# Optimization experiments

Measured on AMD Instinct MI355X. Metric: run time of the kernel, lower is better.

## Reference

```python
import jax, jax.numpy as jnp
import numpy as np

EMBED_DIM = 1024
N_HEADS = 16
DK = EMBED_DIM // N_HEADS


def setup_inputs() -> dict:
    key = jax.random.key(0)
    ks = jax.random.split(key, 9)
    s = 1.0 / np.sqrt(EMBED_DIM)
    d = EMBED_DIM
    return {
        "x": jax.random.normal(ks[0], (2, 2048, d), dtype=jnp.float32),
        "Wq": jax.random.uniform(ks[1], (d, d), jnp.float32, -s, s),
        "bq": jax.random.uniform(ks[2], (d,), jnp.float32, -s, s),
        "Wk": jax.random.uniform(ks[3], (d, d), jnp.float32, -s, s),
        "bk": jax.random.uniform(ks[4], (d,), jnp.float32, -s, s),
        "Wv": jax.random.uniform(ks[5], (d, d), jnp.float32, -s, s),
        "bv": jax.random.uniform(ks[6], (d,), jnp.float32, -s, s),
        "Wo": jax.random.uniform(ks[7], (d, d), jnp.float32, -s, s),
        "bo": jax.random.uniform(ks[8], (d,), jnp.float32, -s, s),
    }


def reference(x, Wq, bq, Wk, bk, Wv, bv, Wo, bo):
    B, S, D = x.shape
    H, dk = N_HEADS, DK
    # QKV projections
    q = (x @ Wq + bq).reshape(B, S, H, dk).transpose(0, 2, 1, 3)  # [B,H,S,dk]
    k = (x @ Wk + bk).reshape(B, S, H, dk).transpose(0, 2, 1, 3)
    v = (x @ Wv + bv).reshape(B, S, H, dk).transpose(0, 2, 1, 3)
    # scaled dot-product attention with full score matrix (faithful to source)
    scores = jnp.einsum("bhqd,bhkd->bhqk", q, k) / jnp.sqrt(jnp.float32(dk))
    attn = jax.nn.softmax(scores, axis=-1)
    out = jnp.einsum("bhqk,bhkd->bhqd", attn, v)  # [B,H,S,dk]
    out = out.transpose(0, 2, 1, 3).reshape(B, S, D)
    return out @ Wo + bo
```

## Files before the change

kernel.cpp:

```cpp
#include <hip/hip_runtime.h>

typedef unsigned short u16;
typedef unsigned int u32;
typedef __attribute__((ext_vector_type(8))) short short8;
typedef __attribute__((ext_vector_type(4))) float float4v;
typedef __attribute__((ext_vector_type(4))) unsigned int uint4v;

struct alignas(8) U16x4 { u16 x, y, z, w; };

__device__ __forceinline__ u16 f2b(float f) {
    union { float f; unsigned int u; } v; v.f = f;
    unsigned int r = (v.u >> 16) & 1u;
    v.u += 0x7fffu + r;
    return (u16)(v.u >> 16);
}

__device__ __forceinline__ float b2f(u16 u) {
    union { unsigned int u; float f; } v; v.u = ((u32)u) << 16; return v.f;
}

__device__ __forceinline__ u32 cvt_pk_bf16(float lo, float hi) {
    u32 d;
    asm("v_cvt_pk_bf16_f32 %0, %1, %2" : "=v"(d) : "v"(lo), "v"(hi));
    return d;
}

__device__ __forceinline__ void gld16(const u16* g, u16* l) {
    __builtin_amdgcn_global_load_lds(
        (const __attribute__((address_space(1))) void*)g,
        (__attribute__((address_space(3))) void*)l, 16, 0, 0);
}

__device__ __forceinline__ short8 frag8(const u16* base, int row, int cg) {
    return *(const short8*)(base + row * 64 + ((cg ^ (row & 7)) << 3));
}

__global__ __launch_bounds__(256) void prep_kernel(
    const float* __restrict__ x, const float* __restrict__ W0,
    const float* __restrict__ W1, const float* __restrict__ W2,
    const float* __restrict__ W3, u16* __restrict__ xb,
    u16* __restrict__ T0, u16* __restrict__ T1,
    u16* __restrict__ T2, u16* __restrict__ T3) {
    __shared__ float tile[32][33];
    int id = blockIdx.x;
    if (id < 4096) {
        size_t i = ((size_t)id * 256 + threadIdx.x) * 4;
        float4 v = *(const float4*)(x + i);
        U16x4 o;
        o.x = f2b(v.x); o.y = f2b(v.y); o.z = f2b(v.z); o.w = f2b(v.w);
        *(U16x4*)(xb + i) = o;
        return;
    }
    int r = id - 4096;
    int z = r >> 10, tl = r & 1023;
    const float* W = (z == 0) ? W0 : (z == 1) ? W1 : (z == 2) ? W2 : W3;
    u16* T = (z == 0) ? T0 : (z == 1) ? T1 : (z == 2) ? T2 : T3;
    int t = threadIdx.x;
    int tx = t & 31, ty = t >> 5;
    int bn = (tl & 31) * 32, bk = (tl >> 5) * 32;
#pragma unroll
    for (int p = 0; p < 4; ++p) {
        int k = ty + p * 8;
        tile[k][tx] = W[(size_t)(bk + k) * 1024 + bn + tx];
    }
    __syncthreads();
#pragma unroll
    for (int p = 0; p < 4; ++p) {
        int n = ty + p * 8;
        T[(size_t)(bn + n) * 1024 + bk + tx] = f2b(tile[tx][n]);
    }
}

__global__ __launch_bounds__(512, 4) void qkv_kernel(
    const u16* __restrict__ X,
    const u16* __restrict__ WqT, const u16* __restrict__ WkT, const u16* __restrict__ WvT,
    const float* __restrict__ bq, const float* __restrict__ bk, const float* __restrict__ bv,
    u16* __restrict__ Qo, u16* __restrict__ Ko, u16* __restrict__ VTo) {
    __shared__ __align__(16) u16 As[64 * 64];
    __shared__ __align__(16) u16 Bs[3][128 * 64];
    int id = blockIdx.x;
    int m = (id & 7) | (((id >> 3) & 7) << 3);
    int n = id >> 6;
    int t = threadIdx.x;
    int m0 = m * 64, n0 = n * 128;
    int lane = t & 63, wid = t >> 6;
    int l16 = lane & 15, quad = lane >> 4;
    int rl = lane >> 3, cs = lane & 7;

    int z_st = (wid - 2) >> 1, half = wid & 1;
    const u16* gsrcB = (z_st == 0) ? WqT : (z_st == 1) ? WkT : WvT;

    float4v acc[3][4];
    float4v zero4 = {0.f, 0.f, 0.f, 0.f};
#pragma unroll
    for (int z = 0; z < 3; ++z)
#pragma unroll
        for (int i = 0; i < 4; ++i) acc[z][i] = zero4;

    for (int k0 = 0; k0 < 1024; k0 += 64) {
        __syncthreads();
        if (wid < 2) {
#pragma unroll
            for (int p = 0; p < 4; ++p) {
                int q = wid * 4 + p;
                int row = q * 8 + rl;
                int c = cs ^ (row & 7);
                gld16(X + (size_t)(m0 + row) * 1024 + k0 + c * 8, As + q * 512);
            }
        } else {
#pragma unroll
            for (int p = 0; p < 8; ++p) {
                int q = half * 8 + p;
                int row = q * 8 + rl;
                int c = cs ^ (row & 7);
                gld16(gsrcB + (size_t)(n0 + row) * 1024 + k0 + c * 8,
                      &Bs[z_st][0] + q * 512);
            }
        }
        __syncthreads();
#pragma unroll
        for (int ks = 0; ks < 64; ks += 32) {
            int cg = (ks >> 3) + quad;
            short8 af[4];
#pragma unroll
            for (int i = 0; i < 4; ++i)
                af[i] = frag8(As, i * 16 + l16, cg);
#pragma unroll
            for (int z = 0; z < 3; ++z) {
                short8 bf = frag8(&Bs[z][0], wid * 16 + l16, cg);
#pragma unroll
                for (int i = 0; i < 4; ++i)
                    acc[z][i] = __builtin_amdgcn_mfma_f32_16x16x32_bf16(
                        af[i], bf, acc[z][i], 0, 0, 0);
            }
        }
    }

    const float QSCALE = 0.18033688011112042f;
    int n1 = n0 + wid * 16 + l16;
    float bql = bq[n1], bkl = bk[n1], bvl = bv[n1];
#pragma unroll
    for (int i = 0; i < 4; ++i) {
        int mbase = m0 + i * 16 + quad * 4;
#pragma unroll
        for (int r = 0; r < 4; ++r) {
            Qo[(size_t)(mbase + r) * 1024 + n1] =
                f2b((acc[0][i][r] + bql) * QSCALE);
            Ko[(size_t)(mbase + r) * 1024 + n1] =
                f2b(acc[1][i][r] + bkl);
        }
        int bidx = mbase >> 11, s = mbase & 2047;
        size_t base =
            ((size_t)((bidx * 16 + (n1 >> 6)) * 64 + (n1 & 63))) * 2048 + s;
        U16x4 pk;
        pk.x = f2b(acc[2][i][0] + bvl);
        pk.y = f2b(acc[2][i][1] + bvl);
        pk.z = f2b(acc[2][i][2] + bvl);
        pk.w = f2b(acc[2][i][3] + bvl);
        *(U16x4*)(VTo + base) = pk;
    }
}

__global__ __launch_bounds__(256, 4) void oproj_kernel(const u16* __restrict__ Op,
                                                       const float* __restrict__ lp,
                                                       const u16* __restrict__ WoT,
                                                       const float* __restrict__ bias,
                                                       float* __restrict__ out) {
    __shared__ __align__(16) u16 As[64 * 64];
    __shared__ __align__(16) u16 Bs[64 * 64];
    __shared__ float invs[64][16];
    int id = blockIdx.x;
    int m = (id & 7) | (((id >> 3) & 7) << 3);
    int n = id >> 6;
    int t = threadIdx.x;
    int m0 = m * 64, n0 = n * 64;
    int lane = t & 63, wid = t >> 6;
    int l16 = lane & 15, quad = lane >> 4;
    int rl = lane >> 3, cs = lane & 7;

#pragma unroll
    for (int e = t; e < 1024; e += 256) {
        int row = e >> 4, h = e & 15;
        int qg = (m0 + row) * 16 + h;
        invs[row][h] = 1.0f / (lp[qg] + lp[65536 + qg]);
    }

    float4v acc[4];
    float4v zero4 = {0.f, 0.f, 0.f, 0.f};
#pragma unroll
    for (int i = 0; i < 4; ++i) acc[i] = zero4;

    for (int k0 = 0; k0 < 1024; k0 += 64) {
        __syncthreads();
#pragma unroll
        for (int p = 0; p < 2; ++p) {
            int blk = wid * 2 + p;
            int row = blk * 8 + rl;
            int c = cs ^ (row & 7);
            gld16(WoT + (size_t)(n0 + row) * 1024 + k0 + c * 8, Bs + blk * 512);
        }
        int h = k0 >> 6;
#pragma unroll
        for (int p = 0; p < 2; ++p) {
            int blk = wid * 2 + p;
            int row = blk * 8 + rl;
            size_t goff = (size_t)(m0 + row) * 1024 + k0 + cs * 8;
            short8 o0 = *(const short8*)(Op + goff);
            short8 o1 = *(const short8*)(Op + 4194304 + goff);
            float iv = invs[row][h];
            uint4v w;
#pragma unroll
            for (int q2 = 0; q2 < 4; ++q2) {
                float a = (b2f((u16)o0[q2 * 2]) + b2f((u16)o1[q2 * 2])) * iv;
                float bb = (b2f((u16)o0[q2 * 2 + 1]) + b2f((u16)o1[q2 * 2 + 1])) * iv;
                w[q2] = cvt_pk_bf16(a, bb);
            }
            *(uint4v*)(As + row * 64 + ((cs ^ (row & 7)) << 3)) = w;
        }
        __syncthreads();
#pragma unroll
        for (int ks = 0; ks < 64; ks += 32) {
            int cg = (ks >> 3) + quad;
            short8 af[4];
#pragma unroll
            for (int i = 0; i < 4; ++i) af[i] = frag8(As, i * 16 + l16, cg);
            short8 bf = frag8(Bs, wid * 16 + l16, cg);
#pragma unroll
            for (int i = 0; i < 4; ++i)
                acc[i] = __builtin_amdgcn_mfma_f32_16x16x32_bf16(
                    af[i], bf, acc[i], 0, 0, 0);
        }
    }

    int n1 = n0 + wid * 16 + l16;
    float bvl = bias[n1];
#pragma unroll
    for (int i = 0; i < 4; ++i) {
        int mbase = m0 + i * 16 + quad * 4;
#pragma unroll
        for (int r = 0; r < 4; ++r)
            out[(size_t)(mbase + r) * 1024 + n1] = acc[i][r] + bvl;
    }
}

__global__ __launch_bounds__(256, 4) void flash_kernel(const u16* __restrict__ Q,
                                                       const u16* __restrict__ Kn,
                                                       const u16* __restrict__ VT,
                                                       u16* __restrict__ Opart,
                                                       float* __restrict__ lpart) {
    __shared__ __align__(16) u16 Ks[2][64 * 64];
    __shared__ __align__(16) u16 Vs[2][64 * 64];

    int id = blockIdx.x;
    int bh = (id & 7) | (((id >> 3) & 3) << 3);
    int rest = id >> 5;
    int qb = rest & 15, kvz = rest >> 4;
    int b = bh >> 4, h = bh & 15;
    int t = threadIdx.x;
    int wid = t >> 6, lane = t & 63;
    int l16 = lane & 15, quad = lane >> 4;
    int rl = lane >> 3, cs = lane & 7;
    int q0 = qb * 128 + wid * 32;
    size_t kbase = (size_t)(b * 2048) * 1024 + h * 64;
    size_t vbase = (size_t)(bh * 64) * 2048;
    int kv0 = kvz * 1024;

    short8 qf[2][2];
#pragma unroll
    for (int j = 0; j < 2; ++j)
#pragma unroll
        for (int kk = 0; kk < 2; ++kk)
            qf[j][kk] = *(const short8*)(
                Q + ((size_t)(b * 2048 + q0 + j * 16 + l16)) * 1024 + h * 64 +
                kk * 32 + quad * 8);

    float4v oacc[2][4];
    float4v den[2];
    float4v zero4 = {0.f, 0.f, 0.f, 0.f};
    const short8 ones8 = {(short)0x3F80, (short)0x3F80, (short)0x3F80, (short)0x3F80,
                          (short)0x3F80, (short)0x3F80, (short)0x3F80, (short)0x3F80};
#pragma unroll
    for (int ip = 0; ip < 2; ++ip) {
        den[ip] = zero4;
#pragma unroll
        for (int jd = 0; jd < 4; ++jd) oacc[ip][jd] = zero4;
    }

#define STAGE_KV(buf, kv)                                                     \
    {                                                                         \
        _Pragma("unroll") for (int p2 = 0; p2 < 2; ++p2) {                    \
            int p = wid * 2 + p2;                                             \
            int row = p * 8 + rl;                                             \
            int c = cs ^ (row & 7);                                           \
            int key = (((row >> 4) & 1) << 5) | (((row >> 2) & 3) << 3) |     \
                      (((row >> 5) & 1) << 2) | (row & 3);                    \
            gld16(Kn + kbase + (size_t)((kv) + key) * 1024 + c * 8,           \
                  &Ks[buf][p * 512]);                                         \
            gld16(VT + vbase + (size_t)row * 2048 + (kv) + c * 8,             \
                  &Vs[buf][p * 512]);                                         \
        }                                                                     \
    }

    STAGE_KV(0, kv0);

    for (int kvi = 0; kvi < 16; ++kvi) {
        int buf = kvi & 1;
        __syncthreads();
        if (kvi + 1 < 16) STAGE_KV(buf ^ 1, kv0 + (kvi + 1) * 64);

        u32 pw[2][4][2];
#pragma unroll
        for (int i = 0; i < 4; ++i) {
            float4v s0 = zero4, s1 = zero4;
            __builtin_amdgcn_s_setprio(1);
#pragma unroll
            for (int kk = 0; kk < 2; ++kk) {
                short8 kf = frag8(&Ks[buf][0], i * 16 + l16, kk * 4 + quad);
                s0 = __builtin_amdgcn_mfma_f32_16x16x32_bf16(kf, qf[0][kk], s0, 0, 0, 0);
                s1 = __builtin_amdgcn_mfma_f32_16x16x32_bf16(kf, qf[1][kk], s1, 0, 0, 0);
            }
            __builtin_amdgcn_s_setprio(0);
#pragma unroll
            for (int j = 0; j < 2; ++j) {
                float4v s = (j == 0) ? s0 : s1;
                float e0f = __builtin_amdgcn_exp2f(s[0]);
                float e1f = __builtin_amdgcn_exp2f(s[1]);
                float e2f = __builtin_amdgcn_exp2f(s[2]);
                float e3f = __builtin_amdgcn_exp2f(s[3]);
                pw[j][i][0] = cvt_pk_bf16(e0f, e1f);
                pw[j][i][1] = cvt_pk_bf16(e2f, e3f);
            }
        }

        __builtin_amdgcn_s_setprio(1);
#pragma unroll
        for (int kk = 0; kk < 2; ++kk) {
            int cg = kk * 4 + quad;
            short8 vf[4];
#pragma unroll
            for (int jd = 0; jd < 4; ++jd)
                vf[jd] = frag8(&Vs[buf][0], jd * 16 + l16, cg);
#pragma unroll
            for (int j = 0; j < 2; ++j) {
                union { uint4v u; short8 s; } pu;
                pu.u = (uint4v){pw[j][kk][0], pw[j][kk][1],
                                pw[j][2 + kk][0], pw[j][2 + kk][1]};
#pragma unroll
                for (int jd = 0; jd < 4; ++jd)
                    oacc[j][jd] = __builtin_amdgcn_mfma_f32_16x16x32_bf16(
                        pu.s, vf[jd], oacc[j][jd], 0, 0, 0);
                den[j] = __builtin_amdgcn_mfma_f32_16x16x32_bf16(
                    pu.s, ones8, den[j], 0, 0, 0);
            }
        }
        __builtin_amdgcn_s_setprio(0);
    }
#undef STAGE_KV

    size_t obase = (size_t)kvz * 4194304;
#pragma unroll
    for (int ip = 0; ip < 2; ++ip)
#pragma unroll
        for (int r = 0; r < 4; ++r) {
            int q = q0 + ip * 16 + quad * 4 + r;
#pragma unroll
            for (int jd = 0; jd < 4; ++jd)
                Opart[obase + ((size_t)(b * 2048 + q)) * 1024 + h * 64 +
                      jd * 16 + l16] = f2b(oacc[ip][jd][r]);
        }
    if (l16 == 0) {
#pragma unroll
        for (int j = 0; j < 2; ++j)
#pragma unroll
            for (int r = 0; r < 4; ++r) {
                int q = q0 + j * 16 + quad * 4 + r;
                lpart[kvz * 65536 + (b * 2048 + q) * 16 + h] = den[j][r];
            }
    }
}

extern "C" void kernel_launch(void* const* d_in, const int* in_sizes, int n_in,
                              void* d_out, int out_size, void* d_ws, size_t ws_size,
                              hipStream_t stream) {
    const float* x  = (const float*)d_in[0];
    const float* Wq = (const float*)d_in[1];
    const float* bq = (const float*)d_in[2];
    const float* Wk = (const float*)d_in[3];
    const float* bk = (const float*)d_in[4];
    const float* Wv = (const float*)d_in[5];
    const float* bv = (const float*)d_in[6];
    const float* Wo = (const float*)d_in[7];
    const float* bo = (const float*)d_in[8];
    float* out = (float*)d_out;

    char* ws = (char*)d_ws;
    const size_t MB = 1024 * 1024;
    u16* xb  = (u16*)(ws);
    u16* wqt = (u16*)(ws + 8 * MB);
    u16* wkt = (u16*)(ws + 10 * MB);
    u16* wvt = (u16*)(ws + 12 * MB);
    u16* wot = (u16*)(ws + 14 * MB);
    u16* qb_ = (u16*)(ws + 16 * MB);
    u16* kb_ = (u16*)(ws + 24 * MB);
    u16* vt_ = (u16*)(ws + 32 * MB);
    u16* op_ = (u16*)(ws + 48 * MB);
    float* lp_ = (float*)(ws + 64 * MB);

    prep_kernel<<<8192, 256, 0, stream>>>(x, Wq, Wk, Wv, Wo, xb,
                                          wqt, wkt, wvt, wot);
    qkv_kernel<<<512, 512, 0, stream>>>(xb, wqt, wkt, wvt, bq, bk, bv,
                                        qb_, kb_, vt_);
    flash_kernel<<<1024, 256, 0, stream>>>(qb_, kb_, vt_, op_, lp_);
    oproj_kernel<<<1024, 256, 0, stream>>>(op_, lp_, wot, bo, out);
}
```

Baseline: 178.3 us.

## Retile QKV GEMM to 128x128 fused weight tiles and prefetch oproj operands

```diff
diff --git a/kernel.cpp b/kernel.cpp
--- a/kernel.cpp
+++ b/kernel.cpp
@@ -71,93 +71,95 @@
     }
 }
 
-__global__ __launch_bounds__(512, 4) void qkv_kernel(
-    const u16* __restrict__ X,
-    const u16* __restrict__ WqT, const u16* __restrict__ WkT, const u16* __restrict__ WvT,
+__global__ __launch_bounds__(256, 3) void qkv_kernel(
+    const u16* __restrict__ X, const u16* __restrict__ WT,
     const float* __restrict__ bq, const float* __restrict__ bk, const float* __restrict__ bv,
     u16* __restrict__ Qo, u16* __restrict__ Ko, u16* __restrict__ VTo) {
-    __shared__ __align__(16) u16 As[64 * 64];
-    __shared__ __align__(16) u16 Bs[3][128 * 64];
+    __shared__ __align__(16) u16 As[128 * 64];
+    __shared__ __align__(16) u16 Bs[128 * 64];
     int id = blockIdx.x;
-    int m = (id & 7) | (((id >> 3) & 7) << 3);
-    int n = id >> 6;
+    int m = (id & 7) | (((id >> 3) & 3) << 3);
+    int n = id >> 5;
     int t = threadIdx.x;
-    int m0 = m * 64, n0 = n * 128;
+    int m0 = m * 128, n0 = n * 128;
     int lane = t & 63, wid = t >> 6;
+    int wr = wid >> 1, wc = wid & 1;
     int l16 = lane & 15, quad = lane >> 4;
     int rl = lane >> 3, cs = lane & 7;
 
-    int z_st = (wid - 2) >> 1, half = wid & 1;
-    const u16* gsrcB = (z_st == 0) ? WqT : (z_st == 1) ? WkT : WvT;
-
-    float4v acc[3][4];
+    const u16* gsrc = (wid < 2) ? X : WT;
+    int gbase = (wid < 2) ? m0 : n0;
+    u16* ldst = (wid < 2) ? As : Bs;
+    int h8 = wid & 1;
+
+    float4v acc[4][4];
     float4v zero4 = {0.f, 0.f, 0.f, 0.f};
 #pragma unroll
-    for (int z = 0; z < 3; ++z)
-#pragma unroll
-        for (int i = 0; i < 4; ++i) acc[z][i] = zero4;
+    for (int i = 0; i < 4; ++i)
+#pragma unroll
+        for (int j = 0; j < 4; ++j) acc[i][j] = zero4;
 
     for (int k0 = 0; k0 < 1024; k0 += 64) {
         __syncthreads();
-        if (wid < 2) {
-#pragma unroll
-            for (int p = 0; p < 4; ++p) {
-                int q = wid * 4 + p;
-                int row = q * 8 + rl;
-                int c = cs ^ (row & 7);
-                gld16(X + (size_t)(m0 + row) * 1024 + k0 + c * 8, As + q * 512);
-            }
-        } else {
-#pragma unroll
-            for (int p = 0; p < 8; ++p) {
-                int q = half * 8 + p;
-                int row = q * 8 + rl;
-                int c = cs ^ (row & 7);
-                gld16(gsrcB + (size_t)(n0 + row) * 1024 + k0 + c * 8,
-                      &Bs[z_st][0] + q * 512);
-            }
+#pragma unroll
+        for (int p = 0; p < 8; ++p) {
+            int q = h8 * 8 + p;
+            int row = q * 8 + rl;
+            int c = cs ^ (row & 7);
+            gld16(gsrc + (size_t)(gbase + row) * 1024 + k0 + c * 8, ldst + q * 512);
         }
         __syncthreads();
 #pragma unroll
         for (int ks = 0; ks < 64; ks += 32) {
             int cg = (ks >> 3) + quad;
-            short8 af[4];
+            short8 af[4], bf[4];
 #pragma unroll
             for (int i = 0; i < 4; ++i)
-                af[i] = frag8(As, i * 16 + l16, cg);
-#pragma unroll
-            for (int z = 0; z < 3; ++z) {
-                short8 bf = frag8(&Bs[z][0], wid * 16 + l16, cg);
-#pragma unroll
-                for (int i = 0; i < 4; ++i)
-                    acc[z][i] = __builtin_amdgcn_mfma_f32_16x16x32_bf16(
-                        af[i], bf, acc[z][i], 0, 0, 0);
-            }
-        }
-    }
-
+                af[i] = frag8(As, wr * 64 + i * 16 + l16, cg);
+#pragma unroll
+            for (int j = 0; j < 4; ++j)
+                bf[j] = frag8(Bs, wc * 64 + j * 16 + l16, cg);
+#pragma unroll
+            for (int i = 0; i < 4; ++i)
+#pragma unroll
+                for (int j = 0; j < 4; ++j)
+                    acc[i][j] = __builtin_amdgcn_mfma_f32_16x16x32_bf16(
+                        af[i], bf[j], acc[i][j], 0, 0, 0);
+        }
+    }
+
+    int z = n >> 3;
     const float QSCALE = 0.18033688011112042f;
-    int n1 = n0 + wid * 16 + l16;
-    float bql = bq[n1], bkl = bk[n1], bvl = bv[n1];
-#pragma unroll
-    for (int i = 0; i < 4; ++i) {
-        int mbase = m0 + i * 16 + quad * 4;
-#pragma unroll
-        for (int r = 0; r < 4; ++r) {
-            Qo[(size_t)(mbase + r) * 1024 + n1] =
-                f2b((acc[0][i][r] + bql) * QSCALE);
-            Ko[(size_t)(mbase + r) * 1024 + n1] =
-                f2b(acc[1][i][r] + bkl);
-        }
-        int bidx = mbase >> 11, s = mbase & 2047;
-        size_t base =
-            ((size_t)((bidx * 16 + (n1 >> 6)) * 64 + (n1 & 63))) * 2048 + s;
-        U16x4 pk;
-        pk.x = f2b(acc[2][i][0] + bvl);
-        pk.y = f2b(acc[2][i][1] + bvl);
-        pk.z = f2b(acc[2][i][2] + bvl);
-        pk.w = f2b(acc[2][i][3] + bvl);
-        *(U16x4*)(VTo + base) = pk;
+#pragma unroll
+    for (int j = 0; j < 4; ++j) {
+        int n1 = n0 + wc * 64 + j * 16 + l16;
+        int col = n1 & 1023;
+        float bcol = (z == 0) ? bq[col] : (z == 1) ? bk[col] : bv[col];
+#pragma unroll
+        for (int i = 0; i < 4; ++i) {
+            int mbase = m0 + wr * 64 + i * 16 + quad * 4;
+            if (z == 0) {
+#pragma unroll
+                for (int r = 0; r < 4; ++r)
+                    Qo[(size_t)(mbase + r) * 1024 + col] =
+                        f2b((acc[i][j][r] + bcol) * QSCALE);
+            } else if (z == 1) {
+#pragma unroll
+                for (int r = 0; r < 4; ++r)
+                    Ko[(size_t)(mbase + r) * 1024 + col] =
+                        f2b(acc[i][j][r] + bcol);
+            } else {
+                int bidx = mbase >> 11, s = mbase & 2047;
+                size_t base =
+                    ((size_t)((bidx * 16 + (col >> 6)) * 64 + (col & 63))) * 2048 + s;
+                U16x4 pk;
+                pk.x = f2b(acc[i][j][0] + bcol);
+                pk.y = f2b(acc[i][j][1] + bcol);
+                pk.z = f2b(acc[i][j][2] + bcol);
+                pk.w = f2b(acc[i][j][3] + bcol);
+                *(U16x4*)(VTo + base) = pk;
+            }
+        }
     }
 }
 
@@ -167,7 +169,7 @@
                                                        const float* __restrict__ bias,
                                                        float* __restrict__ out) {
     __shared__ __align__(16) u16 As[64 * 64];
-    __shared__ __align__(16) u16 Bs[64 * 64];
+    __shared__ __align__(16) u16 Bs[2][64 * 64];
     __shared__ float invs[64][16];
     int id = blockIdx.x;
     int m = (id & 7) | (((id >> 3) & 7) << 3);
@@ -180,51 +182,77 @@
 
 #pragma unroll
     for (int e = t; e < 1024; e += 256) {
-        int row = e >> 4, h = e & 15;
-        int qg = (m0 + row) * 16 + h;
-        invs[row][h] = 1.0f / (lp[qg] + lp[65536 + qg]);
-    }
+        int row = e >> 4, hh = e & 15;
+        int qg = (m0 + row) * 16 + hh;
+        invs[row][hh] = 1.0f / (lp[qg] + lp[65536 + qg]);
+    }
+
+    int row0 = wid * 16 + rl;
+    int row1 = row0 + 8;
+    size_t g0 = (size_t)(m0 + row0) * 1024 + cs * 8;
+    size_t g1 = (size_t)(m0 + row1) * 1024 + cs * 8;
 
     float4v acc[4];
     float4v zero4 = {0.f, 0.f, 0.f, 0.f};
 #pragma unroll
     for (int i = 0; i < 4; ++i) acc[i] = zero4;
 
+#pragma unroll
+    for (int p = 0; p < 2; ++p) {
+        int blk = wid * 2 + p;
+        int row = blk * 8 + rl;
+        int c = cs ^ (row & 7);
+        gld16(WoT + (size_t)(n0 + row) * 1024 + 0 + c * 8, &Bs[0][blk * 512]);
+    }
+    short8 oc00 = *(const short8*)(Op + g0);
+    short8 oc01 = *(const short8*)(Op + 4194304 + g0);
+    short8 oc10 = *(const short8*)(Op + g1);
+    short8 oc11 = *(const short8*)(Op + 4194304 + g1);
+
     for (int k0 = 0; k0 < 1024; k0 += 64) {
+        int buf = (k0 >> 6) & 1;
+        int hh = k0 >> 6;
         __syncthreads();
-#pragma unroll
-        for (int p = 0; p < 2; ++p) {
-            int blk = wid * 2 + p;
-            int row = blk * 8 + rl;
-            int c = cs ^ (row & 7);
-            gld16(WoT + (size_t)(n0 + row) * 1024 + k0 + c * 8, Bs + blk * 512);
-        }
-        int h = k0 >> 6;
-#pragma unroll
-        for (int p = 0; p < 2; ++p) {
-            int blk = wid * 2 + p;
-            int row = blk * 8 + rl;
-            size_t goff = (size_t)(m0 + row) * 1024 + k0 + cs * 8;
-            short8 o0 = *(const short8*)(Op + goff);
-            short8 o1 = *(const short8*)(Op + 4194304 + goff);
-            float iv = invs[row][h];
-            uint4v w;
+
+        {
+            float iv0 = invs[row0][hh], iv1 = invs[row1][hh];
+            uint4v w0, w1;
 #pragma unroll
             for (int q2 = 0; q2 < 4; ++q2) {
-                float a = (b2f((u16)o0[q2 * 2]) + b2f((u16)o1[q2 * 2])) * iv;
-                float bb = (b2f((u16)o0[q2 * 2 + 1]) + b2f((u16)o1[q2 * 2 + 1])) * iv;
-                w[q2] = cvt_pk_bf16(a, bb);
-            }
-            *(uint4v*)(As + row * 64 + ((cs ^ (row & 7)) << 3)) = w;
+                float a0 = (b2f((u16)oc00[q2 * 2]) + b2f((u16)oc01[q2 * 2])) * iv0;
+                float b0 = (b2f((u16)oc00[q2 * 2 + 1]) + b2f((u16)oc01[q2 * 2 + 1])) * iv0;
+                w0[q2] = cvt_pk_bf16(a0, b0);
+                float a1 = (b2f((u16)oc10[q2 * 2]) + b2f((u16)oc11[q2 * 2])) * iv1;
+                float b1 = (b2f((u16)oc10[q2 * 2 + 1]) + b2f((u16)oc11[q2 * 2 + 1])) * iv1;
+                w1[q2] = cvt_pk_bf16(a1, b1);
+            }
+            *(uint4v*)(As + row0 * 64 + ((cs ^ (row0 & 7)) << 3)) = w0;
+            *(uint4v*)(As + row1 * 64 + ((cs ^ (row1 & 7)) << 3)) = w1;
         }
         __syncthreads();
+
+        if (k0 + 64 < 1024) {
+#pragma unroll
+            for (int p = 0; p < 2; ++p) {
+                int blk = wid * 2 + p;
+                int row = blk * 8 + rl;
+                int c = cs ^ (row & 7);
+                gld16(WoT + (size_t)(n0 + row) * 1024 + (k0 + 64) + c * 8,
+                      &Bs[buf ^ 1][blk * 512]);
+            }
+            oc00 = *(const short8*)(Op + g0 + k0 + 64);
+            oc01 = *(const short8*)(Op + 4194304 + g0 + k0 + 64);
+            oc10 = *(const short8*)(Op + g1 + k0 + 64);
+            oc11 = *(const short8*)(Op + 4194304 + g1 + k0 + 64);
+        }
+
 #pragma unroll
         for (int ks = 0; ks < 64; ks += 32) {
             int cg = (ks >> 3) + quad;
             short8 af[4];
 #pragma unroll
             for (int i = 0; i < 4; ++i) af[i] = frag8(As, i * 16 + l16, cg);
-            short8 bf = frag8(Bs, wid * 16 + l16, cg);
+            short8 bf = frag8(&Bs[buf][0], wid * 16 + l16, cg);
 #pragma unroll
             for (int i = 0; i < 4; ++i)
                 acc[i] = __builtin_amdgcn_mfma_f32_16x16x32_bf16(
@@ -408,7 +436,7 @@
 
     prep_kernel<<<8192, 256, 0, stream>>>(x, Wq, Wk, Wv, Wo, xb,
                                           wqt, wkt, wvt, wot);
-    qkv_kernel<<<512, 512, 0, stream>>>(xb, wqt, wkt, wvt, bq, bk, bv,
+    qkv_kernel<<<768, 256, 0, stream>>>(xb, wqt, bq, bk, bv,
                                         qb_, kb_, vt_);
     flash_kernel<<<1024, 256, 0, stream>>>(qb_, kb_, vt_, op_, lp_);
     oproj_kernel<<<1024, 256, 0, stream>>>(op_, lp_, wot, bo, out);
```

New measurement: 183.5 us. 1.03x slower.
